# Optimization experiments

Measured on AMD Instinct MI355X. Metric: run time of the kernel, lower is better.

The kernel has to match this reference:

```python
import jax, jax.numpy as jnp
import numpy as np

N = 100000      # nodes
E = 1600000     # edges (avg degree 16)
F_IN = 14       # Mutagenicity num_node_features
H = 64          # hidden_channels
C = 2           # Mutagenicity num_classes
G = 512         # graphs in batch


def setup_inputs() -> dict:
    key = jax.random.key(0)
    ks = jax.random.split(key, 16)
    x = jax.random.normal(ks[0], (N, F_IN), jnp.float32)
    edge_index = jax.random.randint(ks[1], (2, E), 0, N, dtype=jnp.int32)
    batch = jnp.sort(jax.random.randint(ks[2], (N,), 0, G, dtype=jnp.int32))
    def lin(k, fi, fo):
        bound = 1.0 / np.sqrt(fi)
        kw, kb = jax.random.split(k)
        W = jax.random.uniform(kw, (fi, fo), jnp.float32, -bound, bound)
        b = jax.random.uniform(kb, (fo,), jnp.float32, -bound, bound)
        return W, b
    W1, b1 = lin(ks[3], F_IN, H)
    W2, b2 = lin(ks[4], H, H)
    W3, b3 = lin(ks[5], H, H)
    W4, b4 = lin(ks[6], H, H)
    W5, b5 = lin(ks[7], H, H)
    Wlin, blin = lin(ks[8], H, C)
    return {"x": x, "W1": W1, "b1": b1, "W2": W2, "b2": b2, "W3": W3, "b3": b3,
            "W4": W4, "b4": b4, "W5": W5, "b5": b5, "Wlin": Wlin, "blin": blin,
            "edge_index": edge_index, "batch": batch}


def _gcn_conv(h, W, b, src, dst, norm, dinv):
    # PyG GCNConv: out = D^{-1/2}(A+I)D^{-1/2} (h W) + b
    m = h @ W                                              # [N, Fout]
    agg = jax.ops.segment_sum(m[src] * norm[:, None], dst, num_segments=N)
    agg = agg + m * dinv[:, None]                          # self-loop term (norm = 1/deg)
    return agg + b


def reference(x, W1, b1, W2, b2, W3, b3, W4, b4, W5, b5, Wlin, blin, edge_index, batch):
    src, dst = edge_index[0], edge_index[1]
    # degree with self-loops (counted on target nodes, source_to_target flow)
    deg = jax.ops.segment_sum(jnp.ones(E, jnp.float32), dst, num_segments=N) + 1.0
    dinv_sqrt = jax.lax.rsqrt(deg)
    norm = dinv_sqrt[src] * dinv_sqrt[dst]                 # per-edge weight
    dinv = dinv_sqrt * dinv_sqrt                           # self-loop weight 1/deg

    h = jax.nn.relu(_gcn_conv(x, W1, b1, src, dst, norm, dinv))
    h = jax.nn.relu(_gcn_conv(h, W2, b2, src, dst, norm, dinv))
    h = jax.nn.relu(_gcn_conv(h, W3, b3, src, dst, norm, dinv))
    h = jax.nn.relu(_gcn_conv(h, W4, b4, src, dst, norm, dinv))
    h = jax.nn.relu(_gcn_conv(h, W5, b5, src, dst, norm, dinv))

    pooled = jax.ops.segment_max(h, batch, num_segments=G)  # [G, H]
    return pooled @ Wlin + blin                             # [G, C]
```

## Files before the change

### kernel.cpp

```cpp
#include <hip/hip_runtime.h>
#include <hip/hip_bf16.h>


#define HDIM 64
#define SCAN_CHUNK 1024
#define FILL_S 8


__global__ __launch_bounds__(256) void count_edges(const int* __restrict__ dst,
                                                   int* __restrict__ deg, int E) {
    int e = blockIdx.x * blockDim.x + threadIdx.x;
    if (e < E) atomicAdd(&deg[dst[e]], 1);
}

__global__ __launch_bounds__(256) void partial_sums(const int* __restrict__ deg,
                                                    int* __restrict__ psum, int n) {
    __shared__ int red[256];
    int base = blockIdx.x * SCAN_CHUNK;
    int s = 0;
    #pragma unroll
    for (int j = 0; j < 4; ++j) {
        int i = base + j * 256 + threadIdx.x;
        if (i < n) s += deg[i];
    }
    red[threadIdx.x] = s;
    __syncthreads();
    for (int off = 128; off > 0; off >>= 1) {
        if (threadIdx.x < off) red[threadIdx.x] += red[threadIdx.x + off];
        __syncthreads();
    }
    if (threadIdx.x == 0) psum[blockIdx.x] = red[0];
}

__global__ __launch_bounds__(128) void scan_partials(int* __restrict__ psum, int nb) {
    __shared__ int tmp[128];
    int t = threadIdx.x;
    int v = (t < nb) ? psum[t] : 0;
    tmp[t] = v;
    __syncthreads();
    for (int off = 1; off < 128; off <<= 1) {
        int u = (t >= off) ? tmp[t - off] : 0;
        __syncthreads();
        tmp[t] += u;
        __syncthreads();
    }
    if (t < nb) psum[t] = tmp[t] - v;
}

__global__ __launch_bounds__(256) void scan_final(const int* __restrict__ deg,
                                                  const int* __restrict__ psum,
                                                  int* __restrict__ rowptr, int n) {
    __shared__ int ts[256];
    int t = threadIdx.x;
    int base = blockIdx.x * SCAN_CHUNK + t * 4;
    int v[4];
    int s = 0;
    #pragma unroll
    for (int j = 0; j < 4; ++j) {
        int i = base + j;
        v[j] = (i < n) ? deg[i] : 0;
        s += v[j];
    }
    ts[t] = s;
    __syncthreads();
    int mine = s;
    for (int off = 1; off < 256; off <<= 1) {
        int u = (t >= off) ? ts[t - off] : 0;
        __syncthreads();
        ts[t] += u;
        __syncthreads();
    }
    int ex = ts[t] - mine + psum[blockIdx.x];
    #pragma unroll
    for (int j = 0; j < 4; ++j) {
        int i = base + j;
        if (i < n) rowptr[i] = ex;
        ex += v[j];
    }
}

__global__ __launch_bounds__(256) void node_arrays(const int* __restrict__ deg,
                                                   const int* __restrict__ rowptr,
                                                   float* __restrict__ ds,
                                                   int* __restrict__ cursor, int n) {
    int i = blockIdx.x * blockDim.x + threadIdx.x;
    if (i < n) {
        float d = (float)(deg[i] + 1);
        ds[i] = 1.0f / sqrtf(d);
        cursor[i] = rowptr[i];
    }
}

__global__ __launch_bounds__(256) void fill_csr_sharded(const int* __restrict__ src,
                                                        const int* __restrict__ dst,
                                                        int* __restrict__ cursor,
                                                        int* __restrict__ csr_src,
                                                        int E, int shard_w, int nchunks) {
    int shard = blockIdx.x & (FILL_S - 1);
    int chunk = blockIdx.x >> 3;
    int epc = (E + nchunks - 1) / nchunks;
    int e0 = chunk * epc;
    int e1 = min(e0 + epc, E);
    int lo = shard * shard_w, hi = lo + shard_w;
    for (int e = e0 + (int)threadIdx.x; e < e1; e += 256) {
        int d = dst[e];
        if (d >= lo && d < hi) {
            int pos = atomicAdd(&cursor[d], 1);
            csr_src[pos] = src[e];
        }
    }
}

__global__ __launch_bounds__(256) void pad_scale_x(const float* __restrict__ x,
                                                   const float* __restrict__ ds,
                                                   float* __restrict__ xp, int n_nodes) {
    int idx = blockIdx.x * blockDim.x + threadIdx.x;
    if (idx >= n_nodes * 16) return;
    int n = idx >> 4, j = idx & 15;
    xp[idx] = (j < 14) ? x[n * 14 + j] * ds[n] : 0.0f;
}


__global__ __launch_bounds__(256) void gather16(const float* __restrict__ xp,
                                               const int* __restrict__ rowptr,
                                               const int* __restrict__ cnt,
                                               const int* __restrict__ csr_src,
                                               const float* __restrict__ ds,
                                               float* __restrict__ agg16, int n_nodes) {
    int lane = threadIdx.x & 63;
    int sub = lane >> 4, l = lane & 15;
    int wave = blockIdx.x * (blockDim.x >> 6) + (threadIdx.x >> 6);
    int node = wave * 4 + sub;
    if (node >= n_nodes) return;
    float dsn = ds[node];
    float a0 = xp[node * 16 + l];
    float a1 = 0.f;
    int s = rowptr[node];
    int e = s + cnt[node];
    int i = s;
    for (; i + 1 < e; i += 2) {
        int s0 = csr_src[i], s1 = csr_src[i + 1];
        a0 += xp[s0 * 16 + l];
        a1 += xp[s1 * 16 + l];
    }
    if (i < e) a0 += xp[csr_src[i] * 16 + l];
    agg16[node * 16 + l] = (a0 + a1) * dsn;
}


template <int K, int KW, bool BIAS_RELU, bool SCALE>
__global__ __launch_bounds__(256) void matmul_k(const float* __restrict__ h,
                                                const float* __restrict__ W,
                                                const float* __restrict__ bias,
                                                const float* __restrict__ ds,
                                                float* __restrict__ m, int n_nodes) {
    int lane = threadIdx.x & 63;
    int wave = blockIdx.x * (blockDim.x >> 6) + (threadIdx.x >> 6);
    int n0 = wave * 4;
    if (n0 >= n_nodes) return;
    float wcol[K];
    #pragma unroll
    for (int k = 0; k < K; ++k) wcol[k] = (k < KW) ? W[k * HDIM + lane] : 0.f;
    float bl = BIAS_RELU ? bias[lane] : 0.f;

    if (n0 + 3 < n_nodes) {
        const float4* r0 = reinterpret_cast<const float4*>(h + (size_t)(n0 + 0) * K);
        const float4* r1 = reinterpret_cast<const float4*>(h + (size_t)(n0 + 1) * K);
        const float4* r2 = reinterpret_cast<const float4*>(h + (size_t)(n0 + 2) * K);
        const float4* r3 = reinterpret_cast<const float4*>(h + (size_t)(n0 + 3) * K);
        float a0[4] = {0, 0, 0, 0}, a1[4] = {0, 0, 0, 0};
        float a2[4] = {0, 0, 0, 0}, a3[4] = {0, 0, 0, 0};
        #pragma unroll
        for (int k4 = 0; k4 < K / 4; ++k4) {
            int c = k4 & 3;
            float4 v0 = r0[k4], v1 = r1[k4], v2 = r2[k4], v3 = r3[k4];
            float w0 = wcol[4 * k4 + 0], w1 = wcol[4 * k4 + 1];
            float w2 = wcol[4 * k4 + 2], w3 = wcol[4 * k4 + 3];
            a0[c] += v0.x * w0 + v0.y * w1 + v0.z * w2 + v0.w * w3;
            a1[c] += v1.x * w0 + v1.y * w1 + v1.z * w2 + v1.w * w3;
            a2[c] += v2.x * w0 + v2.y * w1 + v2.z * w2 + v2.w * w3;
            a3[c] += v3.x * w0 + v3.y * w1 + v3.z * w2 + v3.w * w3;
        }
        float s0 = (a0[0] + a0[1]) + (a0[2] + a0[3]);
        float s1 = (a1[0] + a1[1]) + (a1[2] + a1[3]);
        float s2 = (a2[0] + a2[1]) + (a2[2] + a2[3]);
        float s3 = (a3[0] + a3[1]) + (a3[2] + a3[3]);
        if constexpr (BIAS_RELU) {
            s0 = fmaxf(s0 + bl, 0.f);
            s1 = fmaxf(s1 + bl, 0.f);
            s2 = fmaxf(s2 + bl, 0.f);
            s3 = fmaxf(s3 + bl, 0.f);
        }
        if constexpr (SCALE) {
            s0 *= ds[n0 + 0];
            s1 *= ds[n0 + 1];
            s2 *= ds[n0 + 2];
            s3 *= ds[n0 + 3];
        }
        m[(size_t)(n0 + 0) * HDIM + lane] = s0;
        m[(size_t)(n0 + 1) * HDIM + lane] = s1;
        m[(size_t)(n0 + 2) * HDIM + lane] = s2;
        m[(size_t)(n0 + 3) * HDIM + lane] = s3;
    } else {
        for (int n = n0; n < n_nodes; ++n) {
            const float4* hrow = reinterpret_cast<const float4*>(h + (size_t)n * K);
            float acc[4] = {0, 0, 0, 0};
            #pragma unroll
            for (int k4 = 0; k4 < K / 4; ++k4) {
                float4 hv = hrow[k4];
                acc[k4 & 3] += hv.x * wcol[4 * k4 + 0] + hv.y * wcol[4 * k4 + 1] +
                               hv.z * wcol[4 * k4 + 2] + hv.w * wcol[4 * k4 + 3];
            }
            float s = (acc[0] + acc[1]) + (acc[2] + acc[3]);
            if constexpr (BIAS_RELU) s = fmaxf(s + bl, 0.f);
            if constexpr (SCALE) s *= ds[n];
            m[(size_t)n * HDIM + lane] = s;
        }
    }
}


__global__ __launch_bounds__(256) void gcn_gather(const float* __restrict__ m,
                                                  const int* __restrict__ rowptr,
                                                  const int* __restrict__ cnt,
                                                  const int* __restrict__ csr_src,
                                                  const float* __restrict__ ds,
                                                  const float* __restrict__ bias,
                                                  float* __restrict__ hout, int n_nodes) {
    int lane = threadIdx.x & 63;
    int node = blockIdx.x * (blockDim.x >> 6) + (threadIdx.x >> 6);
    if (node >= n_nodes) return;
    float dsn = ds[node];
    float a0 = m[node * HDIM + lane];
    float a1 = 0.f, a2 = 0.f, a3 = 0.f;
    float a4 = 0.f, a5 = 0.f, a6 = 0.f, a7 = 0.f;
    int s = rowptr[node];
    int e = s + cnt[node];
    int i = s;
    for (; i + 7 < e; i += 8) {
        int s0 = csr_src[i],     s1 = csr_src[i + 1], s2 = csr_src[i + 2], s3 = csr_src[i + 3];
        int s4 = csr_src[i + 4], s5 = csr_src[i + 5], s6 = csr_src[i + 6], s7 = csr_src[i + 7];
        a0 += m[s0 * HDIM + lane];
        a1 += m[s1 * HDIM + lane];
        a2 += m[s2 * HDIM + lane];
        a3 += m[s3 * HDIM + lane];
        a4 += m[s4 * HDIM + lane];
        a5 += m[s5 * HDIM + lane];
        a6 += m[s6 * HDIM + lane];
        a7 += m[s7 * HDIM + lane];
    }
    for (; i + 1 < e; i += 2) {
        int s0 = csr_src[i], s1 = csr_src[i + 1];
        a0 += m[s0 * HDIM + lane];
        a1 += m[s1 * HDIM + lane];
    }
    if (i < e) a0 += m[csr_src[i] * HDIM + lane];
    float v = ((a0 + a1) + (a2 + a3) + ((a4 + a5) + (a6 + a7))) * dsn + bias[lane];
    hout[node * HDIM + lane] = fmaxf(v, 0.f);
}


__global__ __launch_bounds__(256) void pool_max(const float* __restrict__ h,
                                                const int* __restrict__ batch,
                                                float* __restrict__ pooled,
                                                int n_nodes, int n_graphs) {
    int lane = threadIdx.x & 63;
    int g = blockIdx.x * (blockDim.x >> 6) + (threadIdx.x >> 6);
    if (g >= n_graphs) return;
    int lo = 0, hi = n_nodes;
    while (lo < hi) { int mid = (lo + hi) >> 1; if (batch[mid] < g) lo = mid + 1; else hi = mid; }
    int start = lo;
    hi = n_nodes;
    while (lo < hi) { int mid = (lo + hi) >> 1; if (batch[mid] < g + 1) lo = mid + 1; else hi = mid; }
    int end = lo;
    float vmax = 0.f;
    for (int n = start; n < end; ++n) vmax = fmaxf(vmax, h[n * HDIM + lane]);
    pooled[g * HDIM + lane] = vmax;
}


__global__ __launch_bounds__(256) void final_linear(const float* __restrict__ pooled,
                                                    const float* __restrict__ Wlin,
                                                    const float* __restrict__ blin,
                                                    float* __restrict__ out, int n_out) {
    int t = blockIdx.x * blockDim.x + threadIdx.x;
    if (t >= n_out) return;
    int g = t >> 1, c = t & 1;
    float acc = blin[c];
    #pragma unroll
    for (int k = 0; k < HDIM; ++k) acc += pooled[g * HDIM + k] * Wlin[k * 2 + c];
    out[t] = acc;
}


extern "C" void kernel_launch(void* const* d_in, const int* in_sizes, int n_in,
                              void* d_out, int out_size, void* d_ws, size_t ws_size,
                              hipStream_t stream) {
    const float* x    = (const float*)d_in[0];
    const float* W1   = (const float*)d_in[1];
    const float* b1   = (const float*)d_in[2];
    const float* W2   = (const float*)d_in[3];
    const float* b2   = (const float*)d_in[4];
    const float* W3   = (const float*)d_in[5];
    const float* b3   = (const float*)d_in[6];
    const float* W4   = (const float*)d_in[7];
    const float* b4   = (const float*)d_in[8];
    const float* W5   = (const float*)d_in[9];
    const float* b5   = (const float*)d_in[10];
    const float* Wlin = (const float*)d_in[11];
    const float* blin = (const float*)d_in[12];
    const int* edge_index = (const int*)d_in[13];
    const int* batch      = (const int*)d_in[14];

    const int N = in_sizes[0] / 14;
    const int E = in_sizes[13] / 2;
    const int G = out_size / 2;
    const int* srcp = edge_index;
    const int* dstp = edge_index + E;

    char* ws = (char*)d_ws;
    size_t off = 0;
    auto alloc = [&](size_t bytes) -> void* {
        void* p = ws + off;
        off = (off + bytes + 255) & ~(size_t)255;
        return p;
    };
    int*   deg     = (int*)alloc((size_t)N * 4);
    int*   rowptr  = (int*)alloc((size_t)N * 4);
    int*   cursor  = (int*)alloc((size_t)N * 4);
    int*   psum    = (int*)alloc(128 * 4);
    float* ds      = (float*)alloc((size_t)N * 4);
    int*   csr_src = (int*)alloc((size_t)E * 4);
    float* buf_m   = (float*)alloc((size_t)N * HDIM * 4);
    float* buf_h   = (float*)alloc((size_t)N * HDIM * 4);
    float* pooled  = (float*)alloc((size_t)G * HDIM * 4);
    (void)ws_size;
    float* xp    = buf_h;
    float* agg16 = buf_m;

    const int NB = (N + SCAN_CHUNK - 1) / SCAN_CHUNK;

    hipMemsetAsync(deg, 0, (size_t)N * 4, stream);
    count_edges<<<(E + 255) / 256, 256, 0, stream>>>(dstp, deg, E);
    partial_sums<<<NB, 256, 0, stream>>>(deg, psum, N);
    scan_partials<<<1, 128, 0, stream>>>(psum, NB);
    scan_final<<<NB, 256, 0, stream>>>(deg, psum, rowptr, N);
    node_arrays<<<(N + 255) / 256, 256, 0, stream>>>(deg, rowptr, ds, cursor, N);
    pad_scale_x<<<(N * 16 + 255) / 256, 256, 0, stream>>>(x, ds, xp, N);

    const int fill_chunks = 512;
    const int shard_w = (N + FILL_S - 1) / FILL_S;
    fill_csr_sharded<<<fill_chunks * FILL_S, 256, 0, stream>>>(srcp, dstp, cursor, csr_src,
                                                               E, shard_w, fill_chunks);

    const int gemm_blocks = (N + 15) / 16;
    const int gather_blocks = (N + 3) / 4;
    const int g16_blocks = (N + 15) / 16;

    gather16<<<g16_blocks, 256, 0, stream>>>(xp, rowptr, deg, csr_src, ds, agg16, N);
    matmul_k<16, 14, true, false><<<gemm_blocks, 256, 0, stream>>>(agg16, W1, b1, ds, buf_h, N);

    matmul_k<64, 64, false, true><<<gemm_blocks, 256, 0, stream>>>(buf_h, W2, b2, ds, buf_m, N);
    gcn_gather<<<gather_blocks, 256, 0, stream>>>(buf_m, rowptr, deg, csr_src, ds, b2, buf_h, N);
    matmul_k<64, 64, false, true><<<gemm_blocks, 256, 0, stream>>>(buf_h, W3, b3, ds, buf_m, N);
    gcn_gather<<<gather_blocks, 256, 0, stream>>>(buf_m, rowptr, deg, csr_src, ds, b3, buf_h, N);
    matmul_k<64, 64, false, true><<<gemm_blocks, 256, 0, stream>>>(buf_h, W4, b4, ds, buf_m, N);
    gcn_gather<<<gather_blocks, 256, 0, stream>>>(buf_m, rowptr, deg, csr_src, ds, b4, buf_h, N);
    matmul_k<64, 64, false, true><<<gemm_blocks, 256, 0, stream>>>(buf_h, W5, b5, ds, buf_m, N);
    gcn_gather<<<gather_blocks, 256, 0, stream>>>(buf_m, rowptr, deg, csr_src, ds, b5, buf_h, N);

    pool_max<<<(G + 3) / 4, 256, 0, stream>>>(buf_h, batch, pooled, N, G);
    final_linear<<<(G * 2 + 255) / 256, 256, 0, stream>>>(pooled, Wlin, blin, (float*)d_out, G * 2);
}
```

Baseline: 834.8 us.

## Build CSR with per-chunk LDS histograms and fuse pooling with final linear

```diff
diff --git a/kernel.cpp b/kernel.cpp
--- a/kernel.cpp
+++ b/kernel.cpp
@@ -5,12 +5,43 @@
 #define HDIM 64
 #define SCAN_CHUNK 1024
 #define FILL_S 8
-
-
-__global__ __launch_bounds__(256) void count_edges(const int* __restrict__ dst,
-                                                   int* __restrict__ deg, int E) {
-    int e = blockIdx.x * blockDim.x + threadIdx.x;
-    if (e < E) atomicAdd(&deg[dst[e]], 1);
+#define C_CHUNKS 32
+#define LDS_BINS 12512
+
+
+__global__ __launch_bounds__(256) void count_sharded(const int* __restrict__ dst,
+                                                     int* __restrict__ counts,
+                                                     int E, int N, int shard_w) {
+    __shared__ int hist[LDS_BINS];
+    int shard = blockIdx.x & (FILL_S - 1);
+    int chunk = blockIdx.x >> 3;
+    int lo = shard * shard_w;
+    int hi = min(lo + shard_w, N);
+    int nb = hi - lo;
+    for (int i = threadIdx.x; i < nb; i += 256) hist[i] = 0;
+    __syncthreads();
+    int epc = (E + C_CHUNKS - 1) / C_CHUNKS;
+    int e0 = chunk * epc, e1 = min(e0 + epc, E);
+    for (int e = e0 + (int)threadIdx.x; e < e1; e += 256) {
+        int d = dst[e];
+        if (d >= lo && d < hi) atomicAdd(&hist[d - lo], 1);
+    }
+    __syncthreads();
+    for (int i = threadIdx.x; i < nb; i += 256) counts[chunk * N + lo + i] = hist[i];
+}
+
+__global__ __launch_bounds__(256) void chunk_scan(int* __restrict__ counts,
+                                                  int* __restrict__ deg, int N) {
+    int n = blockIdx.x * 256 + threadIdx.x;
+    if (n >= N) return;
+    int run = 0;
+    #pragma unroll
+    for (int c = 0; c < C_CHUNKS; ++c) {
+        int t = counts[c * N + n];
+        counts[c * N + n] = run;
+        run += t;
+    }
+    deg[n] = run;
 }
 
 __global__ __launch_bounds__(256) void partial_sums(const int* __restrict__ deg,
@@ -80,32 +111,35 @@
 }
 
 __global__ __launch_bounds__(256) void node_arrays(const int* __restrict__ deg,
-                                                   const int* __restrict__ rowptr,
-                                                   float* __restrict__ ds,
-                                                   int* __restrict__ cursor, int n) {
+                                                   float* __restrict__ ds, int n) {
     int i = blockIdx.x * blockDim.x + threadIdx.x;
     if (i < n) {
         float d = (float)(deg[i] + 1);
         ds[i] = 1.0f / sqrtf(d);
-        cursor[i] = rowptr[i];
-    }
-}
-
-__global__ __launch_bounds__(256) void fill_csr_sharded(const int* __restrict__ src,
-                                                        const int* __restrict__ dst,
-                                                        int* __restrict__ cursor,
-                                                        int* __restrict__ csr_src,
-                                                        int E, int shard_w, int nchunks) {
+    }
+}
+
+__global__ __launch_bounds__(256) void fill_sharded(const int* __restrict__ src,
+                                                    const int* __restrict__ dst,
+                                                    const int* __restrict__ rowptr,
+                                                    const int* __restrict__ counts,
+                                                    int* __restrict__ csr_src,
+                                                    int E, int N, int shard_w) {
+    __shared__ int cur[LDS_BINS];
     int shard = blockIdx.x & (FILL_S - 1);
     int chunk = blockIdx.x >> 3;
-    int epc = (E + nchunks - 1) / nchunks;
-    int e0 = chunk * epc;
-    int e1 = min(e0 + epc, E);
-    int lo = shard * shard_w, hi = lo + shard_w;
+    int lo = shard * shard_w;
+    int hi = min(lo + shard_w, N);
+    int nb = hi - lo;
+    for (int i = threadIdx.x; i < nb; i += 256)
+        cur[i] = rowptr[lo + i] + counts[chunk * N + lo + i];
+    __syncthreads();
+    int epc = (E + C_CHUNKS - 1) / C_CHUNKS;
+    int e0 = chunk * epc, e1 = min(e0 + epc, E);
     for (int e = e0 + (int)threadIdx.x; e < e1; e += 256) {
         int d = dst[e];
         if (d >= lo && d < hi) {
-            int pos = atomicAdd(&cursor[d], 1);
+            int pos = atomicAdd(&cur[d - lo], 1);
             csr_src[pos] = src[e];
         }
     }
@@ -260,10 +294,12 @@
 }
 
 
-__global__ __launch_bounds__(256) void pool_max(const float* __restrict__ h,
-                                                const int* __restrict__ batch,
-                                                float* __restrict__ pooled,
-                                                int n_nodes, int n_graphs) {
+__global__ __launch_bounds__(256) void pool_linear(const float* __restrict__ h,
+                                                   const int* __restrict__ batch,
+                                                   const float* __restrict__ Wlin,
+                                                   const float* __restrict__ blin,
+                                                   float* __restrict__ out,
+                                                   int n_nodes, int n_graphs) {
     int lane = threadIdx.x & 63;
     int g = blockIdx.x * (blockDim.x >> 6) + (threadIdx.x >> 6);
     if (g >= n_graphs) return;
@@ -275,21 +311,17 @@
     int end = lo;
     float vmax = 0.f;
     for (int n = start; n < end; ++n) vmax = fmaxf(vmax, h[n * HDIM + lane]);
-    pooled[g * HDIM + lane] = vmax;
-}
-
-
-__global__ __launch_bounds__(256) void final_linear(const float* __restrict__ pooled,
-                                                    const float* __restrict__ Wlin,
-                                                    const float* __restrict__ blin,
-                                                    float* __restrict__ out, int n_out) {
-    int t = blockIdx.x * blockDim.x + threadIdx.x;
-    if (t >= n_out) return;
-    int g = t >> 1, c = t & 1;
-    float acc = blin[c];
-    #pragma unroll
-    for (int k = 0; k < HDIM; ++k) acc += pooled[g * HDIM + k] * Wlin[k * 2 + c];
-    out[t] = acc;
+    float p0 = vmax * Wlin[lane * 2 + 0];
+    float p1 = vmax * Wlin[lane * 2 + 1];
+    #pragma unroll
+    for (int off = 32; off > 0; off >>= 1) {
+        p0 += __shfl_xor(p0, off);
+        p1 += __shfl_xor(p1, off);
+    }
+    if (lane == 0) {
+        out[g * 2 + 0] = p0 + blin[0];
+        out[g * 2 + 1] = p1 + blin[1];
+    }
 }
 
 
@@ -327,31 +359,28 @@
     };
     int*   deg     = (int*)alloc((size_t)N * 4);
     int*   rowptr  = (int*)alloc((size_t)N * 4);
-    int*   cursor  = (int*)alloc((size_t)N * 4);
     int*   psum    = (int*)alloc(128 * 4);
     float* ds      = (float*)alloc((size_t)N * 4);
     int*   csr_src = (int*)alloc((size_t)E * 4);
     float* buf_m   = (float*)alloc((size_t)N * HDIM * 4);
     float* buf_h   = (float*)alloc((size_t)N * HDIM * 4);
-    float* pooled  = (float*)alloc((size_t)G * HDIM * 4);
     (void)ws_size;
     float* xp    = buf_h;
     float* agg16 = buf_m;
+    int*   counts = (int*)(buf_m + (size_t)N * 16);
 
     const int NB = (N + SCAN_CHUNK - 1) / SCAN_CHUNK;
-
-    hipMemsetAsync(deg, 0, (size_t)N * 4, stream);
-    count_edges<<<(E + 255) / 256, 256, 0, stream>>>(dstp, deg, E);
+    const int shard_w = (N + FILL_S - 1) / FILL_S;
+
+    count_sharded<<<FILL_S * C_CHUNKS, 256, 0, stream>>>(dstp, counts, E, N, shard_w);
+    chunk_scan<<<(N + 255) / 256, 256, 0, stream>>>(counts, deg, N);
     partial_sums<<<NB, 256, 0, stream>>>(deg, psum, N);
     scan_partials<<<1, 128, 0, stream>>>(psum, NB);
     scan_final<<<NB, 256, 0, stream>>>(deg, psum, rowptr, N);
-    node_arrays<<<(N + 255) / 256, 256, 0, stream>>>(deg, rowptr, ds, cursor, N);
+    node_arrays<<<(N + 255) / 256, 256, 0, stream>>>(deg, ds, N);
     pad_scale_x<<<(N * 16 + 255) / 256, 256, 0, stream>>>(x, ds, xp, N);
-
-    const int fill_chunks = 512;
-    const int shard_w = (N + FILL_S - 1) / FILL_S;
-    fill_csr_sharded<<<fill_chunks * FILL_S, 256, 0, stream>>>(srcp, dstp, cursor, csr_src,
-                                                               E, shard_w, fill_chunks);
+    fill_sharded<<<FILL_S * C_CHUNKS, 256, 0, stream>>>(srcp, dstp, rowptr, counts,
+                                                        csr_src, E, N, shard_w);
 
     const int gemm_blocks = (N + 15) / 16;
     const int gather_blocks = (N + 3) / 4;
@@ -369,6 +398,5 @@
     matmul_k<64, 64, false, true><<<gemm_blocks, 256, 0, stream>>>(buf_h, W5, b5, ds, buf_m, N);
     gcn_gather<<<gather_blocks, 256, 0, stream>>>(buf_m, rowptr, deg, csr_src, ds, b5, buf_h, N);
 
-    pool_max<<<(G + 3) / 4, 256, 0, stream>>>(buf_h, batch, pooled, N, G);
-    final_linear<<<(G * 2 + 255) / 256, 256, 0, stream>>>(pooled, Wlin, blin, (float*)d_out, G * 2);
-}
+    pool_linear<<<(G + 3) / 4, 256, 0, stream>>>(buf_h, batch, Wlin, blin, (float*)d_out, N, G);
+}
```

Result: slower. 878.0 us (+5.2%).
